# Optimization experiments

Measured on AMD Instinct MI355X. Metric: run time of the kernel, lower is better.

## Reference

```python
import jax, jax.numpy as jnp
import numpy as np
import math

N_HEADS = 16
D_KV = 64
NUM_BUCKETS = 32
MAX_DISTANCE = 128


def _rel_bucket(rel_pos, num_buckets=NUM_BUCKETS, max_distance=MAX_DISTANCE):
    # bidirectional=True branch of relative_position_bucket
    n = -rel_pos
    num_buckets //= 2
    ret = (n < 0).astype(jnp.int32) * num_buckets
    n = jnp.abs(n)
    max_exact = num_buckets // 2
    is_small = n < max_exact
    val_large = max_exact + (
        jnp.log(n.astype(jnp.float32) / max_exact)
        / math.log(max_distance / max_exact)
        * (num_buckets - max_exact)
    ).astype(jnp.int32)
    val_large = jnp.minimum(val_large, num_buckets - 1)
    return jnp.where(is_small, n, val_large) + ret


def setup_inputs() -> dict:
    key = jax.random.key(0)
    ks = jax.random.split(key, 6)
    T, D = 2048, 1024
    x = jax.random.normal(ks[0], (T, D), dtype=jnp.float32)
    Wq = jax.random.normal(ks[1], (D, N_HEADS * D_KV), dtype=jnp.float32) * 0.02
    Wk = jax.random.normal(ks[2], (D, N_HEADS * D_KV), dtype=jnp.float32) * 0.02
    Wv = jax.random.normal(ks[3], (D, N_HEADS * D_KV), dtype=jnp.float32) * 0.02
    Wo = jax.random.normal(ks[4], (N_HEADS * D_KV, D), dtype=jnp.float32) * 0.02
    rel_bias_table = jax.random.normal(ks[5], (NUM_BUCKETS, N_HEADS), dtype=jnp.float32) * 0.02
    q_lens = jnp.full((4,), 512, dtype=jnp.int32)  # packed varlen: 4 seqs of 512, sum == T
    return {"x": x, "Wq": Wq, "Wk": Wk, "Wv": Wv, "Wo": Wo,
            "rel_bias_table": rel_bias_table, "q_lens": q_lens}


def _attention(x, Wq, Wk, Wv, Wo, rel_bias_table, q_lens):
    T = x.shape[0]
    q = x @ Wq
    k = x @ Wk
    v = x @ Wv
    to_heads = lambda t: jnp.transpose(t.reshape(T, N_HEADS, D_KV), (1, 0, 2))  # [H,T,d]
    q_h, k_h, v_h = to_heads(q), to_heads(k), to_heads(v)

    # fp32 scores (no 1/sqrt(d) scaling in T5; module uses scaling=1.0)
    scores = jnp.einsum('hqd,hkd->hqk', q_h.astype(jnp.float32), k_h.astype(jnp.float32))

    # sequence ids / positions within packed layout
    starts = jnp.cumsum(q_lens, dtype=jnp.int32) - q_lens
    indicators = jnp.zeros(T, dtype=jnp.int32).at[starts].set(1)
    seq_ids = jnp.cumsum(indicators, dtype=jnp.int32) - 1
    pos = jnp.arange(T) - starts[seq_ids]

    # relative position bias (encoder: bidirectional)
    rel_pos = pos[None, :] - pos[:, None]  # [T,T]
    buckets = _rel_bucket(rel_pos)
    bias = jnp.transpose(rel_bias_table[buckets], (2, 0, 1))  # [H,T,T]
    scores = scores + bias.astype(jnp.float32)

    # block-diagonal mask over packed sequences (non-causal encoder)
    total = jnp.sum(q_lens)
    valid = jnp.arange(T) < total
    mask = (seq_ids[:, None] == seq_ids[None, :]) & valid[:, None] & valid[None, :]
    scores = jnp.where(mask[None], scores, jnp.finfo(scores.dtype).min)

    weights = jax.nn.softmax(scores, axis=-1)
    out = jnp.einsum('hqk,hkd->hqd', weights, v_h.astype(jnp.float32))
    out = jnp.transpose(out, (1, 0, 2)).reshape(T, N_HEADS * D_KV)
    return out.astype(x.dtype) @ Wo


def reference(x, Wq, Wk, Wv, Wo, rel_bias_table, q_lens):
    return _attention(x, Wq, Wk, Wv, Wo, rel_bias_table, q_lens)
```

## Files before the change

### kernel.cpp

```cpp
#include <hip/hip_runtime.h>

#define NH 16

typedef __bf16 bf16x8 __attribute__((ext_vector_type(8)));
typedef unsigned short u16x8 __attribute__((ext_vector_type(8)));
typedef float f32x4 __attribute__((ext_vector_type(4)));
typedef unsigned short u16;

__device__ __forceinline__ u16 f2bu(float f) {
    unsigned int u = __builtin_bit_cast(unsigned int, f);
    u = (u + 0x7FFFu + ((u >> 16) & 1u)) >> 16;
    return (u16)u;
}
__device__ __forceinline__ bf16x8 ld_bf8(const u16* p) {
    return __builtin_bit_cast(bf16x8, *(const u16x8*)p);
}
__device__ __forceinline__ void gl_lds16(const void* g, void* l) {
    __builtin_amdgcn_global_load_lds((const __attribute__((address_space(1))) void*)g,
                                     (__attribute__((address_space(3))) void*)l, 16, 0, 0);
}

__device__ __forceinline__ int rel_bucket(int delta) {
    int n = -delta;
    int ret = (n < 0) ? 16 : 0;
    int na = n < 0 ? -n : n;
    int b;
    if (na < 8) b = na;
    else if (na < 12) b = 8;
    else if (na < 16) b = 9;
    else if (na < 23) b = 10;
    else if (na < 32) b = 11;
    else if (na < 46) b = 12;
    else if (na < 64) b = 13;
    else if (na < 91) b = 14;
    else b = 15;
    return b + ret;
}

#define L2E 1.4426950408889634f

__global__ void prep_all(const float* __restrict__ x, u16* __restrict__ xb, int n,
                         const float* __restrict__ Wq, const float* __restrict__ Wk,
                         const float* __restrict__ Wv, const float* __restrict__ Wo,
                         u16* __restrict__ Wt, u16* __restrict__ Wot, int cb) {
    __shared__ float tile[32][33];
    int b = blockIdx.x, tid = threadIdx.x;
    if (b < cb) {
        int i = (b * 256 + tid) * 4;
        if (i >= n) return;
        float4 v = *(const float4*)&x[i];
        u16 o0 = f2bu(v.x), o1 = f2bu(v.y), o2 = f2bu(v.z), o3 = f2bu(v.w);
        xb[i] = o0; xb[i+1] = o1; xb[i+2] = o2; xb[i+3] = o3;
    } else {
        int t = b - cb;
        int z = t >> 10; t &= 1023;
        const float* src = z == 0 ? Wq : z == 1 ? Wk : z == 2 ? Wv : Wo;
        u16* dst = z < 3 ? Wt + (size_t)z * 1024 * 1024 : Wot;
        int r0 = (t >> 5) * 32, c0 = (t & 31) * 32;
        int tx = tid & 31, ty = tid >> 5;
        #pragma unroll
        for (int i = 0; i < 32; i += 8)
            tile[ty + i][tx] = src[(size_t)(r0 + ty + i) * 1024 + c0 + tx];
        __syncthreads();
        #pragma unroll
        for (int i = 0; i < 32; i += 8)
            dst[(size_t)(c0 + ty + i) * 1024 + r0 + tx] = f2bu(tile[tx][ty + i]);
    }
}

template<int MODE, int BM, int XR, int XC>
__global__ __launch_bounds__(256)
void gemm_bt(const u16* __restrict__ A, const u16* __restrict__ Bt,
             int N, int K, int T,
             float* __restrict__ Cf, u16* __restrict__ qkb, u16* __restrict__ vtb) {
    constexpr int MI = BM / 32;
    constexpr int STG = (BM + 128) * 64;
    constexpr int LDSN = (MODE == 1 && 128 * 136 > 2 * STG) ? 128 * 136 : 2 * STG;
    __shared__ __attribute__((aligned(16))) u16 lds[LDSN];
    const int tid = threadIdx.x;
    const int l = tid & 63, wv = tid >> 6;
    const int l16 = l & 15, lg = l >> 4;
    const int lrow = l >> 3, lslot = l & 7;
    const int wm = (wv >> 1) * (BM / 2), wn = (wv & 1) * 64;

    int bmi, bni;
    {
        int gx = gridDim.x, gy = gridDim.y;
        int lin = blockIdx.y * gx + blockIdx.x;
        int nrx = gx / XR, nrc = gy / XC;
        if (gx % XR == 0 && gy % XC == 0 && nrx * nrc == 8) {
            int xcd = lin & 7, loc = lin >> 3;
            int rr = xcd / nrc, rc = xcd % nrc;
            bmi = rr * XR + (loc % XR);
            bni = rc * XC + (loc / XR);
        } else { bmi = blockIdx.x; bni = blockIdx.y; }
    }
    const int bm = bmi * BM, bn = bni * 128;

    f32x4 acc[MI][4];
    #pragma unroll
    for (int i = 0; i < MI; i++)
        #pragma unroll
        for (int j = 0; j < 4; j++)
            #pragma unroll
            for (int r = 0; r < 4; r++) acc[i][j][r] = 0.f;

    auto stage = [&](int k0, int bi) {
        u16* As_ = lds + bi * STG;
        u16* Bs_ = As_ + BM * 64;
        #pragma unroll
        for (int c = 0; c < MI; ++c) {
            int chunk = c * 4 + wv;
            int row = chunk * 8 + lrow;
            int gs = lslot ^ (row & 7);
            gl_lds16(&A[(size_t)(bm + row) * K + k0 + gs * 8], &As_[chunk * 512]);
        }
        #pragma unroll
        for (int c = 0; c < 4; ++c) {
            int chunk = c * 4 + wv;
            int row = chunk * 8 + lrow;
            int gs = lslot ^ (row & 7);
            gl_lds16(&Bt[(size_t)(bn + row) * K + k0 + gs * 8], &Bs_[chunk * 512]);
        }
    };

    stage(0, 0);
    __syncthreads();
    int cur = 0;
    for (int k0 = 0; k0 < K; k0 += 64) {
        if (k0 + 64 < K) stage(k0 + 64, cur ^ 1);
        const u16* As = lds + cur * STG;
        const u16* Bs = As + BM * 64;
        #pragma unroll
        for (int kk = 0; kk < 2; ++kk) {
            bf16x8 af[MI], bfv[4];
            #pragma unroll
            for (int i = 0; i < MI; i++) {
                int row = wm + i * 16 + l16;
                af[i] = ld_bf8(&As[row * 64 + (((kk * 4 + lg) ^ (row & 7)) * 8)]);
            }
            #pragma unroll
            for (int j = 0; j < 4; j++) {
                int row = wn + j * 16 + l16;
                bfv[j] = ld_bf8(&Bs[row * 64 + (((kk * 4 + lg) ^ (row & 7)) * 8)]);
            }
            #pragma unroll
            for (int i = 0; i < MI; i++)
                #pragma unroll
                for (int j = 0; j < 4; j++)
                    acc[i][j] = __builtin_amdgcn_mfma_f32_16x16x32_bf16(af[i], bfv[j], acc[i][j], 0, 0, 0);
        }
        __syncthreads();
        cur ^= 1;
    }

    if (MODE == 0) {
        #pragma unroll
        for (int i = 0; i < MI; i++)
            #pragma unroll
            for (int j = 0; j < 4; j++) {
                int col = bn + wn + j * 16 + l16;
                #pragma unroll
                for (int r = 0; r < 4; r++) {
                    int row = bm + wm + i * 16 + lg * 4 + r;
                    Cf[(size_t)row * N + col] = acc[i][j][r];
                }
            }
    } else if (bn < 2048) {
        #pragma unroll
        for (int i = 0; i < MI; i++)
            #pragma unroll
            for (int j = 0; j < 4; j++) {
                int col = bn + wn + j * 16 + l16;
                #pragma unroll
                for (int r = 0; r < 4; r++) {
                    int row = bm + wm + i * 16 + lg * 4 + r;
                    qkb[(size_t)row * 2048 + col] = f2bu(acc[i][j][r]);
                }
            }
    } else {
        #pragma unroll
        for (int i = 0; i < MI; i++)
            #pragma unroll
            for (int j = 0; j < 4; j++) {
                int cl = wn + j * 16 + l16;
                #pragma unroll
                for (int r = 0; r < 4; r++)
                    lds[cl * 136 + wm + i * 16 + lg * 4 + r] = f2bu(acc[i][j][r]);
            }
        __syncthreads();
        int cl = tid >> 1, hf = tid & 1;
        size_t gb = (size_t)(bn - 2048 + cl) * T + bm + hf * 64;
        #pragma unroll
        for (int k2 = 0; k2 < 8; ++k2) {
            int4 v4 = *(const int4*)&lds[cl * 136 + hf * 64 + k2 * 8];
            *(int4*)&vtb[gb + k2 * 8] = v4;
        }
    }
}

__global__ __launch_bounds__(512)
void attn_kernel(const u16* __restrict__ qkb, const u16* __restrict__ vtb,
                 const float* __restrict__ tbl, const int* __restrict__ q_lens, int nseq,
                 u16* __restrict__ attnb, int T) {
    __shared__ __attribute__((aligned(16))) u16 KV[2][2][4096];
    __shared__ __attribute__((aligned(16))) u16 Ps[8][16][72];
    __shared__ float biasLds[2304];
    const int tid = threadIdx.x;
    const int l = tid & 63, wv = tid >> 6;
    const int l16 = l & 15, lg = l >> 4;
    const int lrow = l >> 3, lslot = l & 7;

    int nbk = gridDim.x * gridDim.y;
    int lin = blockIdx.y * gridDim.x + blockIdx.x;
    int lin2 = (nbk & 7) ? lin : (lin & 7) * (nbk >> 3) + (lin >> 3);
    const int h = lin2 / gridDim.x;
    const int q0 = (lin2 % gridDim.x) * 128;

    int cums[9]; cums[0] = 0;
    #pragma unroll
    for (int i = 0; i < 8; ++i) cums[i + 1] = cums[i] + (i < nseq ? q_lens[i] : 0);
    auto seq_of = [&](int t) -> int {
        int s = -1;
        #pragma unroll
        for (int i = 0; i < 8; ++i)
            if (t >= cums[i] && t < cums[i + 1]) s = i;
        return s;
    };
    const int s0 = seq_of(q0), s1 = seq_of(q0 + 127);
    const bool uni = (s0 == s1) && (s0 >= 0);
    const int kvA = uni ? cums[s0] : 0;
    const int kvB = uni ? cums[s0 + 1] : T;
    const int len = kvB - kvA;

    for (int t = tid; t < len + 128; t += 512)
        biasLds[t] = tbl[rel_bucket(kvA - q0 - 127 + t) * NH + h] * L2E;

    bf16x8 qf[2];
    {
        int tq = q0 + wv * 16 + l16;
        const u16* qp = qkb + (size_t)tq * 2048 + h * 64 + lg * 8;
        qf[0] = ld_bf8(qp); qf[1] = ld_bf8(qp + 32);
    }
    int tqr[4], sqr[4];
    #pragma unroll
    for (int r = 0; r < 4; r++) {
        tqr[r] = q0 + wv * 16 + lg * 4 + r;
        sqr[r] = uni ? s0 : seq_of(tqr[r]);
    }

    const u16* kg = qkb + 1024 + h * 64;
    const u16* vg = vtb + (size_t)(h * 64) * T;
    auto stage = [&](int base, int bi) {
        int row = wv * 8 + lrow;
        int gs = lslot ^ (row & 7);
        int tk = base + row; if (tk > T - 1) tk = T - 1;
        gl_lds16(kg + (size_t)tk * 2048 + gs * 8, &KV[bi][0][wv * 512]);
        gl_lds16(vg + (size_t)row * T + base + gs * 8, &KV[bi][1][wv * 512]);
    };

    float psum[4] = {0.f, 0.f, 0.f, 0.f};
    f32x4 o[4];
    #pragma unroll
    for (int d = 0; d < 4; d++)
        #pragma unroll
        for (int r = 0; r < 4; r++) o[d][r] = 0.f;

    stage(kvA, 0);
    __syncthreads();
    int cur = 0;
    for (int base = kvA; base < kvB; base += 64) {
        if (base + 64 < kvB) stage(base + 64, cur ^ 1);
        const u16* Kb = KV[cur][0];
        const u16* Vb = KV[cur][1];

        f32x4 s[4];
        #pragma unroll
        for (int kt = 0; kt < 4; kt++)
            #pragma unroll
            for (int r = 0; r < 4; r++) s[kt][r] = 0.f;
        #pragma unroll
        for (int kk = 0; kk < 2; kk++)
            #pragma unroll
            for (int kt = 0; kt < 4; kt++) {
                int rw = kt * 16 + l16;
                bf16x8 kf = ld_bf8(Kb + rw * 64 + (((kk * 4 + lg) ^ (rw & 7)) * 8));
                s[kt] = __builtin_amdgcn_mfma_f32_16x16x32_bf16(qf[kk], kf, s[kt], 0, 0, 0);
            }

        const int cbi = (base - kvA) + 127 + l16 - wv * 16 - lg * 4;
        if (uni && base + 64 <= kvB) {
            #pragma unroll
            for (int r = 0; r < 4; r++) {
                const float* bp = &biasLds[cbi - r];
                #pragma unroll
                for (int kt = 0; kt < 4; kt++) {
                    float p = __builtin_amdgcn_exp2f(__builtin_fmaf(s[kt][r], L2E, bp[kt * 16]));
                    psum[r] += p;
                    Ps[wv][lg * 4 + r][kt * 16 + l16] = f2bu(p);
                }
            }
        } else {
            int skt[4];
            #pragma unroll
            for (int kt = 0; kt < 4; kt++) {
                int tk = base + kt * 16 + l16;
                skt[kt] = (tk < T) ? (uni ? s0 : seq_of(tk)) : -2;
            }
            #pragma unroll
            for (int r = 0; r < 4; r++) {
                const float* bp = &biasLds[cbi - r];
                #pragma unroll
                for (int kt = 0; kt < 4; kt++) {
                    float p = __builtin_amdgcn_exp2f(__builtin_fmaf(s[kt][r], L2E, bp[kt * 16]));
                    if (uni) {
                        int tk = base + kt * 16 + l16;
                        if (tk >= kvB) p = 0.f;
                    } else {
                        bool ok = (skt[kt] >= 0) && (skt[kt] == sqr[r]);
                        p = (sqr[r] < 0) ? 1.f : (ok ? p : 0.f);
                    }
                    psum[r] += p;
                    Ps[wv][lg * 4 + r][kt * 16 + l16] = f2bu(p);
                }
            }
        }
        bf16x8 pf0 = ld_bf8(&Ps[wv][l16][lg * 8]);
        bf16x8 pf1 = ld_bf8(&Ps[wv][l16][32 + lg * 8]);
        #pragma unroll
        for (int kk = 0; kk < 2; kk++) {
            bf16x8 pf = kk ? pf1 : pf0;
            #pragma unroll
            for (int dt = 0; dt < 4; dt++) {
                int rw = dt * 16 + l16;
                bf16x8 vf = ld_bf8(Vb + rw * 64 + (((kk * 4 + lg) ^ (rw & 7)) * 8));
                o[dt] = __builtin_amdgcn_mfma_f32_16x16x32_bf16(pf, vf, o[dt], 0, 0, 0);
            }
        }
        __syncthreads();
        cur ^= 1;
    }

    float lsum[4];
    #pragma unroll
    for (int r = 0; r < 4; r++) {
        float v = psum[r];
        #pragma unroll
        for (int m = 1; m < 16; m <<= 1) v += __shfl_xor(v, m, 64);
        lsum[r] = v;
    }
    #pragma unroll
    for (int dt = 0; dt < 4; dt++)
        #pragma unroll
        for (int r = 0; r < 4; r++)
            attnb[(size_t)tqr[r] * 1024 + h * 64 + dt * 16 + l16] = f2bu(o[dt][r] / lsum[r]);
}

extern "C" void kernel_launch(void* const* d_in, const int* in_sizes, int n_in,
                              void* d_out, int out_size, void* d_ws, size_t ws_size,
                              hipStream_t stream) {
    const float* x   = (const float*)d_in[0];
    const float* Wq  = (const float*)d_in[1];
    const float* Wk  = (const float*)d_in[2];
    const float* Wv  = (const float*)d_in[3];
    const float* Wo  = (const float*)d_in[4];
    const float* tbl = (const float*)d_in[5];
    const int* q_lens = (const int*)d_in[6];
    const int T = in_sizes[0] / 1024;
    const int nseq = in_sizes[6];

    char* ws = (char*)d_ws;
    auto alloc = [&](size_t bytes) { char* p = ws; ws += (bytes + 255) & ~(size_t)255; return p; };
    u16*   xb    = (u16*)alloc((size_t)T * 1024 * 2);
    u16*   Wt    = (u16*)alloc((size_t)3072 * 1024 * 2);
    u16*   Wot   = (u16*)alloc((size_t)1024 * 1024 * 2);
    u16*   qkb   = (u16*)alloc((size_t)T * 2048 * 2);
    u16*   vtb   = (u16*)alloc((size_t)1024 * T * 2);
    u16*   attnb = (u16*)alloc((size_t)T * 1024 * 2);

    int cb = (T * 1024 / 4 + 255) / 256;
    prep_all<<<dim3(cb + 4096), dim3(256), 0, stream>>>(
        x, xb, T * 1024, Wq, Wk, Wv, Wo, Wt, Wot, cb);

    gemm_bt<1, 128, 8, 6><<<dim3(T / 128, 3072 / 128), dim3(256), 0, stream>>>(
        xb, Wt, 3072, 1024, T, nullptr, qkb, vtb);
    attn_kernel<<<dim3(T / 128, NH), dim3(512), 0, stream>>>(
        qkb, vtb, tbl, q_lens, nseq, attnb, T);
    gemm_bt<0, 64, 8, 4><<<dim3(T / 64, 1024 / 128), dim3(256), 0, stream>>>(
        attnb, Wot, 1024, 1024, T, (float*)d_out, nullptr, nullptr);
}
```

Before: 129.0 us.

## Split attention over KV chunks into partial sums with a separate reduce kernel

Replaces the single attention kernel with a split-KV version. Each block now handles 64 queries and one quarter of the sequence's keys in 128-key tiles, writing unnormalized fp32 partial outputs and row sums. A new reduce kernel combines them and normalizes to bf16. This raises the block count to fill more compute units, but adds a large fp32 intermediate write/read, an extra launch, and drops the double-buffered K/V prefetch.

```diff
diff --git a/kernel.cpp b/kernel.cpp
--- a/kernel.cpp
+++ b/kernel.cpp
@@ -1,9 +1,11 @@
 #include <hip/hip_runtime.h>
 
 #define NH 16
+#define NSPLIT 4
 
 typedef __bf16 bf16x8 __attribute__((ext_vector_type(8)));
 typedef unsigned short u16x8 __attribute__((ext_vector_type(8)));
+typedef unsigned short u16x4 __attribute__((ext_vector_type(4)));
 typedef float f32x4 __attribute__((ext_vector_type(4)));
 typedef unsigned short u16;
 
@@ -199,23 +201,21 @@
     }
 }
 
-__global__ __launch_bounds__(512)
-void attn_kernel(const u16* __restrict__ qkb, const u16* __restrict__ vtb,
-                 const float* __restrict__ tbl, const int* __restrict__ q_lens, int nseq,
-                 u16* __restrict__ attnb, int T) {
-    __shared__ __attribute__((aligned(16))) u16 KV[2][2][4096];
-    __shared__ __attribute__((aligned(16))) u16 Ps[8][16][72];
-    __shared__ float biasLds[2304];
+__global__ __launch_bounds__(256)
+void attn_part(const u16* __restrict__ qkb, const u16* __restrict__ vtb,
+               const float* __restrict__ tbl, const int* __restrict__ q_lens, int nseq,
+               float* __restrict__ op, float* __restrict__ ps, int T) {
+    __shared__ __attribute__((aligned(16))) u16 KP[8704];
+    __shared__ __attribute__((aligned(16))) u16 Vs[8192];
+    __shared__ float biasC[192];
     const int tid = threadIdx.x;
     const int l = tid & 63, wv = tid >> 6;
     const int l16 = l & 15, lg = l >> 4;
     const int lrow = l >> 3, lslot = l & 7;
 
-    int nbk = gridDim.x * gridDim.y;
-    int lin = blockIdx.y * gridDim.x + blockIdx.x;
-    int lin2 = (nbk & 7) ? lin : (lin & 7) * (nbk >> 3) + (lin >> 3);
-    const int h = lin2 / gridDim.x;
-    const int q0 = (lin2 % gridDim.x) * 128;
+    const int h = blockIdx.y;
+    const int q0 = blockIdx.x * 64;
+    const int sp = blockIdx.z;
 
     int cums[9]; cums[0] = 0;
     #pragma unroll
@@ -227,14 +227,13 @@
             if (t >= cums[i] && t < cums[i + 1]) s = i;
         return s;
     };
-    const int s0 = seq_of(q0), s1 = seq_of(q0 + 127);
+    const int s0 = seq_of(q0), s1 = seq_of(q0 + 63);
     const bool uni = (s0 == s1) && (s0 >= 0);
     const int kvA = uni ? cums[s0] : 0;
     const int kvB = uni ? cums[s0 + 1] : T;
-    const int len = kvB - kvA;
-
-    for (int t = tid; t < len + 128; t += 512)
-        biasLds[t] = tbl[rel_bucket(kvA - q0 - 127 + t) * NH + h] * L2E;
+    const int clen = (kvB - kvA + NSPLIT - 1) / NSPLIT;
+    const int ck0 = kvA + sp * clen;
+    const int ce = min(ck0 + clen, kvB);
 
     bf16x8 qf[2];
     {
@@ -251,13 +250,6 @@
 
     const u16* kg = qkb + 1024 + h * 64;
     const u16* vg = vtb + (size_t)(h * 64) * T;
-    auto stage = [&](int base, int bi) {
-        int row = wv * 8 + lrow;
-        int gs = lslot ^ (row & 7);
-        int tk = base + row; if (tk > T - 1) tk = T - 1;
-        gl_lds16(kg + (size_t)tk * 2048 + gs * 8, &KV[bi][0][wv * 512]);
-        gl_lds16(vg + (size_t)row * T + base + gs * 8, &KV[bi][1][wv * 512]);
-    };
 
     float psum[4] = {0.f, 0.f, 0.f, 0.f};
     f32x4 o[4];
@@ -266,94 +258,123 @@
         #pragma unroll
         for (int r = 0; r < 4; r++) o[d][r] = 0.f;
 
-    stage(kvA, 0);
-    __syncthreads();
-    int cur = 0;
-    for (int base = kvA; base < kvB; base += 64) {
-        if (base + 64 < kvB) stage(base + 64, cur ^ 1);
-        const u16* Kb = KV[cur][0];
-        const u16* Vb = KV[cur][1];
-
-        f32x4 s[4];
-        #pragma unroll
-        for (int kt = 0; kt < 4; kt++)
+    const int cbi = 63 + l16 - wv * 16 - lg * 4;
+
+    for (int kb = ck0; kb < ce; kb += 128) {
+        if (kb > ck0) __syncthreads();
+        if (tid < 192) biasC[tid] = tbl[rel_bucket(tid - 63 + (kb - q0)) * NH + h] * L2E;
+        #pragma unroll
+        for (int c = 0; c < 4; ++c) {
+            int chunk = c * 4 + wv;
+            int row = chunk * 8 + lrow;
+            int gs = lslot ^ (row & 7);
+            int tk = kb + row; if (tk > T - 1) tk = T - 1;
+            gl_lds16(kg + (size_t)tk * 2048 + gs * 8, &KP[chunk * 512]);
+        }
+        #pragma unroll
+        for (int c = 0; c < 4; ++c) {
+            int chunk = c * 4 + wv;
+            int vrow = chunk * 4 + (l >> 4);
+            int gs = l16 ^ (vrow & 15);
+            gl_lds16(vg + (size_t)vrow * T + kb + gs * 8, &Vs[chunk * 512]);
+        }
+        __syncthreads();
+
+        f32x4 s[8];
+        #pragma unroll
+        for (int kt = 0; kt < 8; kt++)
             #pragma unroll
             for (int r = 0; r < 4; r++) s[kt][r] = 0.f;
         #pragma unroll
         for (int kk = 0; kk < 2; kk++)
             #pragma unroll
-            for (int kt = 0; kt < 4; kt++) {
+            for (int kt = 0; kt < 8; kt++) {
                 int rw = kt * 16 + l16;
-                bf16x8 kf = ld_bf8(Kb + rw * 64 + (((kk * 4 + lg) ^ (rw & 7)) * 8));
+                bf16x8 kf = ld_bf8(&KP[rw * 64 + (((kk * 4 + lg) ^ (rw & 7)) * 8)]);
                 s[kt] = __builtin_amdgcn_mfma_f32_16x16x32_bf16(qf[kk], kf, s[kt], 0, 0, 0);
             }
-
-        const int cbi = (base - kvA) + 127 + l16 - wv * 16 - lg * 4;
-        if (uni && base + 64 <= kvB) {
+        __syncthreads();
+
+        if (uni && kb + 128 <= ce) {
             #pragma unroll
             for (int r = 0; r < 4; r++) {
-                const float* bp = &biasLds[cbi - r];
-                #pragma unroll
-                for (int kt = 0; kt < 4; kt++) {
+                const float* bp = &biasC[cbi - r];
+                #pragma unroll
+                for (int kt = 0; kt < 8; kt++) {
                     float p = __builtin_amdgcn_exp2f(__builtin_fmaf(s[kt][r], L2E, bp[kt * 16]));
                     psum[r] += p;
-                    Ps[wv][lg * 4 + r][kt * 16 + l16] = f2bu(p);
+                    KP[(wv * 16 + lg * 4 + r) * 136 + kt * 16 + l16] = f2bu(p);
                 }
             }
         } else {
-            int skt[4];
-            #pragma unroll
-            for (int kt = 0; kt < 4; kt++) {
-                int tk = base + kt * 16 + l16;
-                skt[kt] = (tk < T) ? (uni ? s0 : seq_of(tk)) : -2;
+            int skt[8];
+            #pragma unroll
+            for (int kt = 0; kt < 8; kt++) {
+                int tk = kb + kt * 16 + l16;
+                skt[kt] = (tk < ce) ? (uni ? s0 : seq_of(tk)) : -2;
             }
             #pragma unroll
             for (int r = 0; r < 4; r++) {
-                const float* bp = &biasLds[cbi - r];
-                #pragma unroll
-                for (int kt = 0; kt < 4; kt++) {
+                const float* bp = &biasC[cbi - r];
+                #pragma unroll
+                for (int kt = 0; kt < 8; kt++) {
                     float p = __builtin_amdgcn_exp2f(__builtin_fmaf(s[kt][r], L2E, bp[kt * 16]));
                     if (uni) {
-                        int tk = base + kt * 16 + l16;
-                        if (tk >= kvB) p = 0.f;
+                        if (kb + kt * 16 + l16 >= ce) p = 0.f;
                     } else {
                         bool ok = (skt[kt] >= 0) && (skt[kt] == sqr[r]);
-                        p = (sqr[r] < 0) ? 1.f : (ok ? p : 0.f);
+                        p = (sqr[r] < 0) ? ((skt[kt] != -2) ? 1.f : 0.f) : (ok ? p : 0.f);
                     }
                     psum[r] += p;
-                    Ps[wv][lg * 4 + r][kt * 16 + l16] = f2bu(p);
+                    KP[(wv * 16 + lg * 4 + r) * 136 + kt * 16 + l16] = f2bu(p);
                 }
             }
         }
-        bf16x8 pf0 = ld_bf8(&Ps[wv][l16][lg * 8]);
-        bf16x8 pf1 = ld_bf8(&Ps[wv][l16][32 + lg * 8]);
-        #pragma unroll
-        for (int kk = 0; kk < 2; kk++) {
-            bf16x8 pf = kk ? pf1 : pf0;
+        #pragma unroll
+        for (int kk = 0; kk < 4; kk++) {
+            bf16x8 pf = ld_bf8(&KP[(wv * 16 + l16) * 136 + kk * 32 + lg * 8]);
             #pragma unroll
             for (int dt = 0; dt < 4; dt++) {
                 int rw = dt * 16 + l16;
-                bf16x8 vf = ld_bf8(Vb + rw * 64 + (((kk * 4 + lg) ^ (rw & 7)) * 8));
+                bf16x8 vf = ld_bf8(&Vs[rw * 128 + (((kk * 4 + lg) ^ (rw & 15)) * 8)]);
                 o[dt] = __builtin_amdgcn_mfma_f32_16x16x32_bf16(pf, vf, o[dt], 0, 0, 0);
             }
         }
-        __syncthreads();
-        cur ^= 1;
-    }
-
-    float lsum[4];
+    }
+
     #pragma unroll
     for (int r = 0; r < 4; r++) {
         float v = psum[r];
         #pragma unroll
         for (int m = 1; m < 16; m <<= 1) v += __shfl_xor(v, m, 64);
-        lsum[r] = v;
+        if (l16 == 0) ps[((size_t)sp * T + tqr[r]) * NH + h] = v;
     }
     #pragma unroll
     for (int dt = 0; dt < 4; dt++)
         #pragma unroll
         for (int r = 0; r < 4; r++)
-            attnb[(size_t)tqr[r] * 1024 + h * 64 + dt * 16 + l16] = f2bu(o[dt][r] / lsum[r]);
+            op[((size_t)sp * T + tqr[r]) * 1024 + h * 64 + dt * 16 + l16] = o[dt][r];
+}
+
+__global__ __launch_bounds__(256)
+void attn_reduce(const float* __restrict__ op, const float* __restrict__ ps,
+                 u16* __restrict__ attnb, int T) {
+    int t = blockIdx.x, j = threadIdx.x;
+    int h = j >> 4;
+    f32x4 a = {0.f, 0.f, 0.f, 0.f};
+    float den = 0.f;
+    #pragma unroll
+    for (int sp = 0; sp < NSPLIT; ++sp) {
+        const float* pp = &op[((size_t)sp * T + t) * 1024 + j * 4];
+        f32x4 v = *(const f32x4*)pp;
+        a += v;
+        den += ps[((size_t)sp * T + t) * NH + h];
+    }
+    float inv = 1.f / den;
+    u16x4 outv;
+    #pragma unroll
+    for (int e = 0; e < 4; ++e) outv[e] = f2bu(a[e] * inv);
+    *(u16x4*)&attnb[(size_t)t * 1024 + j * 4] = outv;
 }
 
 extern "C" void kernel_launch(void* const* d_in, const int* in_sizes, int n_in,
@@ -377,6 +398,8 @@
     u16*   qkb   = (u16*)alloc((size_t)T * 2048 * 2);
     u16*   vtb   = (u16*)alloc((size_t)1024 * T * 2);
     u16*   attnb = (u16*)alloc((size_t)T * 1024 * 2);
+    float* op    = (float*)alloc((size_t)NSPLIT * T * 1024 * 4);
+    float* ps    = (float*)alloc((size_t)NSPLIT * T * NH * 4);
 
     int cb = (T * 1024 / 4 + 255) / 256;
     prep_all<<<dim3(cb + 4096), dim3(256), 0, stream>>>(
@@ -384,8 +407,9 @@
 
     gemm_bt<1, 128, 8, 6><<<dim3(T / 128, 3072 / 128), dim3(256), 0, stream>>>(
         xb, Wt, 3072, 1024, T, nullptr, qkb, vtb);
-    attn_kernel<<<dim3(T / 128, NH), dim3(512), 0, stream>>>(
-        qkb, vtb, tbl, q_lens, nseq, attnb, T);
+    attn_part<<<dim3(T / 64, NH, NSPLIT), dim3(256), 0, stream>>>(
+        qkb, vtb, tbl, q_lens, nseq, op, ps, T);
+    attn_reduce<<<dim3(T), dim3(256), 0, stream>>>(op, ps, attnb, T);
     gemm_bt<0, 64, 8, 4><<<dim3(T / 64, 1024 / 128), dim3(256), 0, stream>>>(
         attnb, Wot, 1024, 1024, T, (float*)d_out, nullptr, nullptr);
 }
```

New measurement: 146.3 us. 1.13x slower.
